# Kernel optimization log

Hardware: AMD Instinct MI355X
Metric: run time of the kernel (lower is better)

The kernel has to match this reference:

```python
import jax, jax.numpy as jnp
import numpy as np

N_QUBITS = 12
Q_DEPTH = 3
N_GEN = 2
BATCH = 4096
TEMPERATURE = 5.0
DATA_REUPLOADING = False
DIM = 2 ** N_QUBITS


def setup_inputs() -> dict:
    key = jax.random.key(0)
    k1, k2, k3, k4 = jax.random.split(key, 4)
    x = jax.random.uniform(k1, (BATCH, N_QUBITS), jnp.float32) * (np.pi / 2)
    q_params = jax.random.uniform(k2, (N_GEN, Q_DEPTH * N_QUBITS * 3), jnp.float32)  # q_delta=1
    lin_w = jax.random.normal(k3, (DIM, N_QUBITS), jnp.float32) / np.sqrt(N_QUBITS)
    lin_b = jax.random.normal(k4, (DIM,), jnp.float32) * 0.01
    valid_state_mask = jnp.ones((DIM,), jnp.float32)
    return {"x": x, "q_params": q_params, "lin_w": lin_w, "lin_b": lin_b,
            "valid_state_mask": valid_state_mask}


def _ry(t):
    c, s = jnp.cos(t / 2), jnp.sin(t / 2)
    m = jnp.stack([jnp.stack([c, -s], -1), jnp.stack([s, c], -1)], -2)
    return m.astype(jnp.complex64)


def _rx(t):
    c = jnp.cos(t / 2).astype(jnp.complex64)
    s = (-1j) * jnp.sin(t / 2).astype(jnp.complex64)
    return jnp.stack([jnp.stack([c, s], -1), jnp.stack([s, c], -1)], -2)


def _rz(t):
    e = jnp.exp(-0.5j * t.astype(jnp.complex64))
    z = jnp.zeros_like(e)
    return jnp.stack([jnp.stack([e, z], -1), jnp.stack([z, jnp.conj(e)], -1)], -2)


def _apply_1q(state, U, wire):
    # state: (B, 2, 2, ..., 2); U: (2,2) shared or (B,2,2) per-sample
    ax = 1 + wire
    s = jnp.moveaxis(state, ax, -1)
    if U.ndim == 3:
        s = jnp.einsum('b...i,bji->b...j', s, U)
    else:
        s = jnp.einsum('...i,ji->...j', s, U)
    return jnp.moveaxis(s, -1, ax)


def _cnot(state, c, t):
    s = jnp.moveaxis(state, (1 + c, 1 + t), (1, 2))
    s = jnp.stack([s[:, 0], s[:, 1, ::-1]], axis=1)  # flip target where control=1
    return jnp.moveaxis(s, (1, 2), (1 + c, 1 + t))


def _circuit_probs(x, weights):
    # x: (B, n_qubits) noise; weights: (q_depth*n_qubits*3,)
    B = x.shape[0]
    state = jnp.zeros((B,) + (2,) * N_QUBITS, jnp.complex64)
    state = state.at[(slice(None),) + (0,) * N_QUBITS].set(1.0)
    w = weights.reshape(Q_DEPTH, N_QUBITS * 3)
    for i in range(Q_DEPTH):
        if DATA_REUPLOADING or i == 0:
            for j in range(N_QUBITS):
                state = _apply_1q(state, _ry(x[:, j]), j)
        for y in range(N_QUBITS):
            state = _apply_1q(state, _rz(w[i, 3 * y]), y)
            state = _apply_1q(state, _rx(w[i, 3 * y + 1]), y)
            state = _apply_1q(state, _ry(w[i, 3 * y + 2]), y)
        for y in range(N_QUBITS - 1):
            state = _cnot(state, y, y + 1)
        state = _cnot(state, N_QUBITS - 1, 0)  # python for-else always runs
    amp = state.reshape(B, DIM)
    return (amp.real ** 2 + amp.imag ** 2).astype(jnp.float32)


def reference(x, q_params, lin_w, lin_b, valid_state_mask):
    outputs = jnp.concatenate([_circuit_probs(x, q_params[g]) for g in range(N_GEN)], axis=1)
    converted_x = (x @ lin_w.T + lin_b) * TEMPERATURE
    return outputs, converted_x
```

## Files before the change

kernel.cpp:

```cpp
#include <hip/hip_runtime.h>

#define NQ     12
#define DIM    4096
#define BATCH  4096
#define NGEN   2

typedef float f32x2 __attribute__((ext_vector_type(2)));

constexpr unsigned cnot_map(unsigned b, int c, int t) {
  return b ^ (((b >> c) & 1u) << t);
}
constexpr unsigned ring_fwd(unsigned b) {
  b = cnot_map(b, 0, 11);
  for (int y = 10; y >= 0; --y) b = cnot_map(b, 11 - y, 10 - y);
  return b;
}
constexpr unsigned ring_inv(unsigned b) {
  for (int y = 0; y <= 10; ++y) b = cnot_map(b, 11 - y, 10 - y);
  b = cnot_map(b, 0, 11);
  return b;
}
constexpr unsigned pw (unsigned b, int k) { for (int r = 0; r < k; ++r) b = ring_fwd(b); return b; }
constexpr unsigned pwi(unsigned b, int k) { for (int r = 0; r < k; ++r) b = ring_inv(b); return b; }
constexpr int parity12(unsigned x) { int p = 0; for (int j = 0; j < 12; ++j) p ^= (x >> j) & 1; return p; }

struct QT {
  unsigned short v[2][12];
  unsigned short c[2][12];
};
constexpr QT make_qt() {
  QT t{};
  for (int li = 0; li < 2; ++li)
    for (int y = 0; y < 12; ++y) {
      const int p = 11 - y;
      t.v[li][y] = (unsigned short)pw(1u << p, li + 1);
      unsigned cm = 0;
      for (int j = 0; j < 12; ++j)
        cm |= (unsigned)((pwi(1u << j, li + 1) >> p) & 1u) << j;
      t.c[li][y] = (unsigned short)cm;
    }
  return t;
}
constexpr QT qt = make_qt();

constexpr bool ortho_ok() {
  for (int li = 0; li < 2; ++li)
    for (int a = 0; a < 12; ++a)
      for (int b = 0; b < 12; ++b)
        if (parity12((unsigned)qt.v[li][a] & (unsigned)qt.c[li][b]) != (a == b ? 1 : 0))
          return false;
  if (ring_inv(ring_fwd(0xABCu)) != 0xABCu) return false;
  return true;
}
static_assert(ortho_ok(), "GF(2) orthogonality violated");

constexpr unsigned A12(unsigned q) { return (q ^ (q >> 4) ^ (q >> 8)) & 0xFFFu; }

constexpr int msb12(unsigned x) { int m = -1; for (int i = 0; i < 12; ++i) if ((x >> i) & 1) m = i; return m; }
constexpr bool bins(unsigned* byMsb, unsigned x) {
  while (x) { int m = msb12(x); if (!byMsb[m]) { byMsb[m] = x; return true; } x ^= byMsb[m]; }
  return false;
}

struct GTab {
  unsigned lut[6][256];
  unsigned short gv[6][16];
  unsigned short sflo[256];
  unsigned short sfhi[16];
  unsigned char ok;
};
constexpr GTab make_gtab() {
  GTab t{};
  bool good = true;
  for (int li = 0; li < 2; ++li)
    for (int gi = 0; gi < 3; ++gi) {
      const int gid = li * 3 + gi;
      unsigned v[4], cm[4];
      for (int b = 0; b < 4; ++b) { v[b] = qt.v[li][gi * 4 + b]; cm[b] = qt.c[li][gi * 4 + b]; }
      unsigned byMsb[12] = {};
      for (int b = 0; b < 4; ++b) if (!bins(byMsb, v[b])) good = false;
      int Tpos[8] = {}; int c = 0;
      for (int cand = 0; cand < 12 && c < 8; ++cand)
        if (bins(byMsb, 1u << cand)) Tpos[c++] = cand;
      if (c != 8) good = false;
      for (int tid = 0; tid < 256; ++tid) {
        unsigned q = 0;
        for (int cc = 0; cc < 8; ++cc) if ((tid >> cc) & 1) q ^= 1u << Tpos[cc];
        unsigned pb = 0;
        for (int b = 0; b < 4; ++b) pb |= (unsigned)parity12(q & cm[b]) << b;
        t.lut[gid][tid] = (pb << 16) | (A12(q) << 3);
      }
      for (int j = 0; j < 16; ++j) {
        unsigned g = 0;
        for (int b = 0; b < 4; ++b) if ((j >> b) & 1) g ^= v[b];
        t.gv[gid][j] = (unsigned short)A12(g);
      }
      bool seen[4096] = {};
      for (int tid = 0; tid < 256; ++tid)
        for (int j = 0; j < 16; ++j) {
          unsigned idx = ((t.lut[gid][tid] & 0xFFFFu) >> 3) ^ (unsigned)t.gv[gid][j];
          if (idx >= 4096 || seen[idx]) good = false;
          seen[idx] = true;
        }
    }
  for (int tid = 0; tid < 256; ++tid) t.sflo[tid] = (unsigned short)A12(pw((unsigned)tid, 3));
  for (int k = 0; k < 16; ++k)       t.sfhi[k]   = (unsigned short)A12(pw((unsigned)k << 8, 3));
  t.ok = good ? 1 : 0;
  return t;
}
constexpr GTab h_gtab = make_gtab();
static_assert(h_gtab.ok == 1, "group tables inconsistent");
__constant__ GTab d_gtab = make_gtab();

__device__ __forceinline__ float2 cmuls(float2 a, float2 b) {
  return make_float2(a.x * b.x - a.y * b.y, a.x * b.y + a.y * b.x);
}
__device__ __forceinline__ float2 cadds(float2 a, float2 b) {
  return make_float2(a.x + b.x, a.y + b.y);
}
__device__ __forceinline__ void mat2mul(const float2* A, const float2* B, float2* C) {
  C[0] = cadds(cmuls(A[0], B[0]), cmuls(A[1], B[2]));
  C[1] = cadds(cmuls(A[0], B[1]), cmuls(A[1], B[3]));
  C[2] = cadds(cmuls(A[2], B[0]), cmuls(A[3], B[2]));
  C[3] = cadds(cmuls(A[2], B[1]), cmuls(A[3], B[3]));
}
__device__ __forceinline__ void fusedU(float a, float b, float c, float2* U) {
  float sa, ca, sb, cb, sc, cc;
  sincosf(a * 0.5f, &sa, &ca);
  sincosf(b * 0.5f, &sb, &cb);
  sincosf(c * 0.5f, &sc, &cc);
  float2 RZ[4] = { {ca, -sa}, {0.f, 0.f}, {0.f, 0.f}, {ca, sa} };
  float2 RX[4] = { {cb, 0.f}, {0.f, -sb}, {0.f, -sb}, {cb, 0.f} };
  float2 RY[4] = { {cc, 0.f}, {-sc, 0.f}, {sc, 0.f}, {cc, 0.f} };
  float2 M[4];
  mat2mul(RX, RZ, M);
  mat2mul(RY, M, U);
}

__device__ __forceinline__ f32x2 pcmul(f32x2 a, f32x2 b) {
  return (f32x2){a.x, a.x} * b + (f32x2){-a.y, a.y} * (f32x2){b.y, b.x};
}
__device__ __forceinline__ float xorf(float f, unsigned m) {
  return __uint_as_float(__float_as_uint(f) ^ m);
}

template<int GID>
__device__ __forceinline__ void do_pass(f32x2* st, const f32x2 (*gAB)[2], int tid) {
  const unsigned L   = d_gtab.lut[GID][tid];
  const unsigned tbB = L & 0xFFFFu;
  const unsigned pb  = L >> 16;
  char* stb = (char*)st;

  f32x2 e[16];
  #pragma unroll
  for (int j = 0; j < 16; ++j)
    e[j] = *(const f32x2*)(stb + (tbB ^ ((unsigned)h_gtab.gv[GID][j] << 3)));

  constexpr int gbase = (GID / 3) * 12 + (GID % 3) * 4;
  #pragma unroll
  for (int b = 0; b < 4; ++b) {
    const f32x2 ga = gAB[gbase + b][0];
    const f32x2 gb = gAB[gbase + b][1];
    const unsigned sg = ((pb >> b) & 1u) << 31;
    const float ax = ga.x;
    const float ay = xorf(ga.y, sg);
    const float bx = xorf(gb.x, sg);
    const float by = gb.y;
    const f32x2 P1 = {ax, ax};
    const f32x2 P2 = {-ay, ay};
    const f32x2 P3 = {bx, bx};
    const f32x2 P4 = {-by, by};
    #pragma unroll
    for (int j0 = 0; j0 < 16; ++j0) {
      if (j0 & (1 << b)) continue;
      const int j1 = j0 | (1 << b);
      const f32x2 s0 = e[j0], s1 = e[j1];
      const f32x2 w0 = {s0.y, s0.x}, w1 = {s1.y, s1.x};
      e[j0] = P1 * s0 + P2 * w0 + P3 * s1 + P4 * w1;
      e[j1] = P1 * s1 - P2 * w1 - P3 * s0 + P4 * w0;
    }
  }
  #pragma unroll
  for (int j = 0; j < 16; ++j)
    *(f32x2*)(stb + (tbB ^ ((unsigned)h_gtab.gv[GID][j] << 3))) = e[j];
}

__global__ __launch_bounds__(256, 4) void qcirc_kernel(const float* __restrict__ x,
                                                       const float* __restrict__ qp,
                                                       float* __restrict__ out) {
  __shared__ f32x2 st[DIM];
  __shared__ f32x2 gAB[24][2];
  __shared__ f32x2 vq[NQ][2];

  const int tid = threadIdx.x;
  const int s = blockIdx.x >> 1;
  const int g = blockIdx.x & 1;

  if (tid < 24) {
    const int li = tid / 12, y = tid % 12;
    const float* w = qp + g * 108 + (li + 1) * 36 + 3 * y;
    float2 U[4];
    fusedU(w[0], w[1], w[2], U);
    gAB[tid][0] = (f32x2){U[0].x, U[0].y};
    gAB[tid][1] = (f32x2){U[1].x, U[1].y};
  } else if (tid >= 64 && tid < 64 + NQ) {
    const int j = tid - 64;
    const float* w = qp + g * 108 + 3 * j;
    float2 U0[4];
    fusedU(w[0], w[1], w[2], U0);
    float cx, sx;
    sincosf(x[s * NQ + j] * 0.5f, &sx, &cx);
    vq[j][0] = (f32x2){U0[0].x * cx + U0[1].x * sx, U0[0].y * cx + U0[1].y * sx};
    vq[j][1] = (f32x2){U0[2].x * cx + U0[3].x * sx, U0[2].y * cx + U0[3].y * sx};
  }
  __syncthreads();

  {
    const unsigned bt = (unsigned)tid ^ ((unsigned)tid >> 4);
    f32x2 low = vq[11][tid & 1];
    #pragma unroll
    for (int p = 1; p < 8; ++p) low = pcmul(low, vq[11 - p][(tid >> p) & 1]);
    #pragma unroll
    for (int r = 0; r < 16; ++r) {
      f32x2 h = vq[3][r & 1];
      h = pcmul(h, vq[2][(r >> 1) & 1]);
      h = pcmul(h, vq[1][(r >> 2) & 1]);
      h = pcmul(h, vq[0][(r >> 3) & 1]);
      st[(r * 0x111) ^ bt] = pcmul(low, h);
    }
  }

  __syncthreads(); do_pass<0>(st, gAB, tid);
  __syncthreads(); do_pass<1>(st, gAB, tid);
  __syncthreads(); do_pass<2>(st, gAB, tid);
  __syncthreads(); do_pass<3>(st, gAB, tid);
  __syncthreads(); do_pass<4>(st, gAB, tid);
  __syncthreads(); do_pass<5>(st, gAB, tid);
  __syncthreads();

  float* ob = out + (size_t)s * (NGEN * DIM) + (size_t)g * DIM;
  const unsigned lo = d_gtab.sflo[tid];
  #pragma unroll
  for (int k = 0; k < 16; ++k) {
    const f32x2 a = st[lo ^ d_gtab.sfhi[k]];
    ob[k * 256 + tid] = a.x * a.x + a.y * a.y;
  }
}

#define SPB 8
__global__ __launch_bounds__(256) void linear_kernel(const float* __restrict__ x,
                                                     const float* __restrict__ w,
                                                     const float* __restrict__ bb,
                                                     float* __restrict__ out2) {
  __shared__ float xs[SPB * NQ];
  const int tid = threadIdx.x;
  const int d0 = (blockIdx.x & 3) * 1024 + tid * 4;
  const int s0 = (blockIdx.x >> 2) * SPB;

  if (tid < SPB * NQ / 4)
    ((float4*)xs)[tid] = ((const float4*)(x + (size_t)s0 * NQ))[tid];

  float wr[4][NQ];
  float b4[4];
  #pragma unroll
  for (int dd = 0; dd < 4; ++dd) {
    #pragma unroll
    for (int jj = 0; jj < 3; ++jj)
      *(float4*)&wr[dd][jj * 4] = *(const float4*)&w[(size_t)(d0 + dd) * NQ + jj * 4];
    b4[dd] = bb[d0 + dd];
  }
  __syncthreads();

  #pragma unroll
  for (int s = 0; s < SPB; ++s) {
    float4 r;
    float* rp = &r.x;
    #pragma unroll
    for (int dd = 0; dd < 4; ++dd) {
      float acc = b4[dd];
      #pragma unroll
      for (int j = 0; j < NQ; ++j) acc = fmaf(xs[s * NQ + j], wr[dd][j], acc);
      rp[dd] = acc * 5.0f;
    }
    *(float4*)&out2[(size_t)(s0 + s) * DIM + d0] = r;
  }
}

extern "C" void kernel_launch(void* const* d_in, const int* in_sizes, int n_in,
                              void* d_out, int out_size, void* d_ws, size_t ws_size,
                              hipStream_t stream) {
  const float* x    = (const float*)d_in[0];
  const float* qp   = (const float*)d_in[1];
  const float* linw = (const float*)d_in[2];
  const float* linb = (const float*)d_in[3];
  float* out = (float*)d_out;

  qcirc_kernel<<<BATCH * NGEN, 256, 0, stream>>>(x, qp, out);
  linear_kernel<<<(BATCH / SPB) * 4, 256, 0, stream>>>(x, linw, linb,
                                                       out + (size_t)BATCH * NGEN * DIM);
}
```

Measured before the change: 343.1 us.

## Fuse linear projection into circuit kernel and hand-code packed FMA butterflies

The separate linear kernel is removed. Each circuit block now also computes half of the linear output row for its sample: x is loaded into registers and the weight rows are read straight from global memory. The 2x2 complex butterfly is rewritten with inline v_pk_mul/v_pk_fma using op_sel and neg modifiers, so operand swizzles and negations need no separate instructions. LUT entries and sflo are preloaded into registers up front. This drops one launch and cuts ALU work in the hot passes, at the cost of extra registers and redundant weight loads in every block.

```diff
diff --git a/kernel.cpp b/kernel.cpp
--- a/kernel.cpp
+++ b/kernel.cpp
@@ -144,9 +144,44 @@
   return __uint_as_float(__float_as_uint(f) ^ m);
 }
 
+__device__ __forceinline__ f32x2 pk_mul_dl(f32x2 a, f32x2 b) {
+  f32x2 d;
+  asm("v_pk_mul_f32 %0, %1, %2 op_sel:[0,0] op_sel_hi:[0,1]" : "=v"(d) : "v"(a), "v"(b));
+  return d;
+}
+__device__ __forceinline__ f32x2 pk_f1(f32x2 a, f32x2 s, f32x2 c) {
+  f32x2 d;
+  asm("v_pk_fma_f32 %0, %1, %2, %3 op_sel:[0,1,0] op_sel_hi:[0,0,1] neg_lo:[1,0,0]"
+      : "=v"(d) : "v"(a), "v"(s), "v"(c));
+  return d;
+}
+__device__ __forceinline__ f32x2 pk_f1b(f32x2 a, f32x2 s, f32x2 c) {
+  f32x2 d;
+  asm("v_pk_fma_f32 %0, %1, %2, %3 op_sel:[0,1,0] op_sel_hi:[0,0,1] neg_hi:[1,0,0]"
+      : "=v"(d) : "v"(a), "v"(s), "v"(c));
+  return d;
+}
+__device__ __forceinline__ f32x2 pk_f2(f32x2 a, f32x2 s, f32x2 c) {
+  f32x2 d;
+  asm("v_pk_fma_f32 %0, %1, %2, %3 op_sel:[1,0,0] op_sel_hi:[1,1,1]"
+      : "=v"(d) : "v"(a), "v"(s), "v"(c));
+  return d;
+}
+__device__ __forceinline__ f32x2 pk_f2b(f32x2 a, f32x2 s, f32x2 c) {
+  f32x2 d;
+  asm("v_pk_fma_f32 %0, %1, %2, %3 op_sel:[1,0,0] op_sel_hi:[1,1,1] neg_lo:[1,0,0] neg_hi:[1,0,0]"
+      : "=v"(d) : "v"(a), "v"(s), "v"(c));
+  return d;
+}
+__device__ __forceinline__ f32x2 pk_f3(f32x2 a, f32x2 s, f32x2 c) {
+  f32x2 d;
+  asm("v_pk_fma_f32 %0, %1, %2, %3 op_sel:[1,1,0] op_sel_hi:[1,0,1] neg_lo:[1,0,0]"
+      : "=v"(d) : "v"(a), "v"(s), "v"(c));
+  return d;
+}
+
 template<int GID>
-__device__ __forceinline__ void do_pass(f32x2* st, const f32x2 (*gAB)[2], int tid) {
-  const unsigned L   = d_gtab.lut[GID][tid];
+__device__ __forceinline__ void do_pass(f32x2* st, const f32x2 (*gAB)[2], unsigned L) {
   const unsigned tbB = L & 0xFFFFu;
   const unsigned pb  = L >> 16;
   char* stb = (char*)st;
@@ -162,22 +197,24 @@
     const f32x2 ga = gAB[gbase + b][0];
     const f32x2 gb = gAB[gbase + b][1];
     const unsigned sg = ((pb >> b) & 1u) << 31;
-    const float ax = ga.x;
-    const float ay = xorf(ga.y, sg);
-    const float bx = xorf(gb.x, sg);
-    const float by = gb.y;
-    const f32x2 P1 = {ax, ax};
-    const f32x2 P2 = {-ay, ay};
-    const f32x2 P3 = {bx, bx};
-    const f32x2 P4 = {-by, by};
+    f32x2 q;
+    q.x = xorf(ga.y, sg);
+    q.y = xorf(gb.x, sg);
     #pragma unroll
     for (int j0 = 0; j0 < 16; ++j0) {
       if (j0 & (1 << b)) continue;
       const int j1 = j0 | (1 << b);
       const f32x2 s0 = e[j0], s1 = e[j1];
-      const f32x2 w0 = {s0.y, s0.x}, w1 = {s1.y, s1.x};
-      e[j0] = P1 * s0 + P2 * w0 + P3 * s1 + P4 * w1;
-      e[j1] = P1 * s1 - P2 * w1 - P3 * s0 + P4 * w0;
+      f32x2 t0 = pk_mul_dl(ga, s0);
+      t0 = pk_f1(q, s0, t0);
+      t0 = pk_f2(q, s1, t0);
+      t0 = pk_f3(gb, s1, t0);
+      f32x2 t1 = pk_mul_dl(ga, s1);
+      t1 = pk_f1b(q, s1, t1);
+      t1 = pk_f2b(q, s0, t1);
+      t1 = pk_f3(gb, s0, t1);
+      e[j0] = t0;
+      e[j1] = t1;
     }
   }
   #pragma unroll
@@ -187,6 +224,8 @@
 
 __global__ __launch_bounds__(256, 4) void qcirc_kernel(const float* __restrict__ x,
                                                        const float* __restrict__ qp,
+                                                       const float* __restrict__ lw,
+                                                       const float* __restrict__ lb,
                                                        float* __restrict__ out) {
   __shared__ f32x2 st[DIM];
   __shared__ f32x2 gAB[24][2];
@@ -195,6 +234,15 @@
   const int tid = threadIdx.x;
   const int s = blockIdx.x >> 1;
   const int g = blockIdx.x & 1;
+
+  unsigned lutr[6];
+  #pragma unroll
+  for (int i = 0; i < 6; ++i) lutr[i] = d_gtab.lut[i][tid];
+  const unsigned sflo = d_gtab.sflo[tid];
+  float xr[NQ];
+  #pragma unroll
+  for (int jj = 0; jj < 3; ++jj)
+    *(float4*)&xr[jj * 4] = *(const float4*)&x[s * NQ + jj * 4];
 
   if (tid < 24) {
     const int li = tid / 12, y = tid % 12;
@@ -230,59 +278,38 @@
     }
   }
 
-  __syncthreads(); do_pass<0>(st, gAB, tid);
-  __syncthreads(); do_pass<1>(st, gAB, tid);
-  __syncthreads(); do_pass<2>(st, gAB, tid);
-  __syncthreads(); do_pass<3>(st, gAB, tid);
-  __syncthreads(); do_pass<4>(st, gAB, tid);
-  __syncthreads(); do_pass<5>(st, gAB, tid);
+  __syncthreads(); do_pass<0>(st, gAB, lutr[0]);
+  __syncthreads(); do_pass<1>(st, gAB, lutr[1]);
+  __syncthreads(); do_pass<2>(st, gAB, lutr[2]);
+  __syncthreads(); do_pass<3>(st, gAB, lutr[3]);
+  __syncthreads(); do_pass<4>(st, gAB, lutr[4]);
+  __syncthreads(); do_pass<5>(st, gAB, lutr[5]);
   __syncthreads();
 
   float* ob = out + (size_t)s * (NGEN * DIM) + (size_t)g * DIM;
-  const unsigned lo = d_gtab.sflo[tid];
   #pragma unroll
   for (int k = 0; k < 16; ++k) {
-    const f32x2 a = st[lo ^ d_gtab.sfhi[k]];
+    const f32x2 a = st[(sflo ^ (unsigned)h_gtab.sfhi[k])];
     ob[k * 256 + tid] = a.x * a.x + a.y * a.y;
   }
-}
-
-#define SPB 8
-__global__ __launch_bounds__(256) void linear_kernel(const float* __restrict__ x,
-                                                     const float* __restrict__ w,
-                                                     const float* __restrict__ bb,
-                                                     float* __restrict__ out2) {
-  __shared__ float xs[SPB * NQ];
-  const int tid = threadIdx.x;
-  const int d0 = (blockIdx.x & 3) * 1024 + tid * 4;
-  const int s0 = (blockIdx.x >> 2) * SPB;
-
-  if (tid < SPB * NQ / 4)
-    ((float4*)xs)[tid] = ((const float4*)(x + (size_t)s0 * NQ))[tid];
-
-  float wr[4][NQ];
-  float b4[4];
-  #pragma unroll
-  for (int dd = 0; dd < 4; ++dd) {
-    #pragma unroll
-    for (int jj = 0; jj < 3; ++jj)
-      *(float4*)&wr[dd][jj * 4] = *(const float4*)&w[(size_t)(d0 + dd) * NQ + jj * 4];
-    b4[dd] = bb[d0 + dd];
-  }
-  __syncthreads();
-
-  #pragma unroll
-  for (int s = 0; s < SPB; ++s) {
+
+  float* o2 = out + (size_t)BATCH * NGEN * DIM + (size_t)s * DIM;
+  #pragma unroll
+  for (int it = 0; it < 2; ++it) {
+    const int d0 = g * 2048 + it * 1024 + tid * 4;
+    const float4 b4 = *(const float4*)&lb[d0];
     float4 r;
     float* rp = &r.x;
+    const float* bp = &b4.x;
     #pragma unroll
     for (int dd = 0; dd < 4; ++dd) {
-      float acc = b4[dd];
+      float acc = bp[dd];
+      const float* wrow = lw + (size_t)(d0 + dd) * NQ;
       #pragma unroll
-      for (int j = 0; j < NQ; ++j) acc = fmaf(xs[s * NQ + j], wr[dd][j], acc);
+      for (int j = 0; j < NQ; ++j) acc = fmaf(xr[j], wrow[j], acc);
       rp[dd] = acc * 5.0f;
     }
-    *(float4*)&out2[(size_t)(s0 + s) * DIM + d0] = r;
+    *(float4*)&o2[d0] = r;
   }
 }
 
@@ -295,7 +322,5 @@
   const float* linb = (const float*)d_in[3];
   float* out = (float*)d_out;
 
-  qcirc_kernel<<<BATCH * NGEN, 256, 0, stream>>>(x, qp, out);
-  linear_kernel<<<(BATCH / SPB) * 4, 256, 0, stream>>>(x, linw, linb,
-                                                       out + (size_t)BATCH * NGEN * DIM);
-}
+  qcirc_kernel<<<BATCH * NGEN, 256, 0, stream>>>(x, qp, linw, linb, out);
+}
```

Measured after the change: 353.2 us. +2.9%, slower.
